# Kernel tuning notes

Measured on AMD Instinct MI355X. Metric: run time of the kernel, lower is better.

Reference implementation:

```python
import jax, jax.numpy as jnp
import numpy as np

N_HEAD = 16
N_KV_HEAD = 4
HEAD_DIM = 128
EPS = 1e-6


def apply_rotary_emb(x, cos, sin):
    # x: (B,T,H,hd); cos/sin: (1,T,1,hd//2)
    d = x.shape[3] // 2
    x1, x2 = x[..., :d], x[..., d:]
    y1 = x1 * cos + x2 * sin
    y2 = x1 * -sin + x2 * cos
    return jnp.concatenate([y1, y2], axis=3).astype(x.dtype)


def rmsnorm(x):
    # flax nnx.RMSNorm with use_scale=False: x * rsqrt(mean(x^2) + eps)
    ms = jnp.mean(jnp.square(x), axis=-1, keepdims=True)
    return (x * jax.lax.rsqrt(ms + EPS)).astype(x.dtype)


def setup_inputs() -> dict:
    key = jax.random.key(0)
    ks = jax.random.split(key, 7)
    B, T, C = 4, 2048, 2048
    s = 0.02
    return {
        "x": jax.random.normal(ks[0], (B, T, C), jnp.float32),
        "cos": jax.random.normal(ks[1], (1, T, 1, HEAD_DIM // 2), jnp.float32),
        "sin": jax.random.normal(ks[2], (1, T, 1, HEAD_DIM // 2), jnp.float32),
        "Wq": jax.random.normal(ks[3], (C, N_HEAD * HEAD_DIM), jnp.float32) * s,
        "Wk": jax.random.normal(ks[4], (C, N_KV_HEAD * HEAD_DIM), jnp.float32) * s,
        "Wv": jax.random.normal(ks[5], (C, N_KV_HEAD * HEAD_DIM), jnp.float32) * s,
        "Wo": jax.random.normal(ks[6], (C, C), jnp.float32) * s,
    }


def reference(x, cos, sin, Wq, Wk, Wv, Wo):
    B, T, C = x.shape
    q = (x @ Wq).reshape(B, T, N_HEAD, HEAD_DIM)
    k = (x @ Wk).reshape(B, T, N_KV_HEAD, HEAD_DIM)
    v = (x @ Wv).reshape(B, T, N_KV_HEAD, HEAD_DIM)
    q = rmsnorm(apply_rotary_emb(q, cos, sin))
    k = rmsnorm(apply_rotary_emb(k, cos, sin))
    # (B,H,T,hd)
    q = jnp.transpose(q, (0, 2, 1, 3))
    k = jnp.transpose(k, (0, 2, 1, 3))
    v = jnp.transpose(v, (0, 2, 1, 3))
    nrep = N_HEAD // N_KV_HEAD
    k = jnp.repeat(k, nrep, axis=1)
    v = jnp.repeat(v, nrep, axis=1)
    scale = 1.0 / jnp.sqrt(jnp.float32(HEAD_DIM))
    att = jnp.einsum('bhqd,bhkd->bhqk', q, k) * scale
    mask = jnp.tril(jnp.ones((T, T), dtype=bool))[None, None, :, :]
    att = jnp.where(mask, att, -jnp.inf)
    att = jax.nn.softmax(att, axis=-1)
    y = jnp.einsum('bhqk,bhkd->bhqd', att, v)
    y = jnp.transpose(y, (0, 2, 1, 3)).reshape(B, T, -1)
    return y @ Wo
```

## Files before the change

kernel.cpp:

```cpp
#include <hip/hip_runtime.h>
#include <hip/hip_bf16.h>

typedef __attribute__((ext_vector_type(8))) short short8;
typedef __attribute__((ext_vector_type(4))) float f32x4;

#define B_SZ 4
#define T_SEQ 2048
#define C_DIM 2048
#define NH 16
#define NKV 4
#define HD 128

__device__ __forceinline__ unsigned short f2bf(float f) {
  union { __hip_bfloat16 h; unsigned short u; } v;
  v.h = __float2bfloat16(f);
  return v.u;
}
__device__ __forceinline__ float bf2f(unsigned short u) {
  union { unsigned short u; __hip_bfloat16 h; } v;
  v.u = u;
  return __bfloat162float(v.h);
}

__device__ __forceinline__ void gload_lds16(const unsigned short* g, unsigned short* l) {
  __builtin_amdgcn_global_load_lds(
      (const __attribute__((address_space(1))) unsigned int*)g,
      (__attribute__((address_space(3))) unsigned int*)l, 16, 0, 0);
}

__global__ void cast_x(const float* __restrict__ x, unsigned short* __restrict__ xb, int n4) {
  int i = blockIdx.x * blockDim.x + threadIdx.x;
  if (i < n4) {
    float4 f = ((const float4*)x)[i];
    ushort4 u = make_ushort4(f2bf(f.x), f2bf(f.y), f2bf(f.z), f2bf(f.w));
    ((ushort4*)xb)[i] = u;
  }
}

__global__ void wtrans(const float* __restrict__ W, unsigned short* __restrict__ Wt, int K, int N) {
  __shared__ float tile[32][33];
  int k0 = blockIdx.x * 32, n0 = blockIdx.y * 32;
  int tx = threadIdx.x, ty = threadIdx.y;
#pragma unroll
  for (int i = 0; i < 4; i++)
    tile[ty + i * 8][tx] = W[(size_t)(k0 + ty + i * 8) * N + n0 + tx];
  __syncthreads();
#pragma unroll
  for (int i = 0; i < 4; i++)
    Wt[(size_t)(n0 + ty + i * 8) * K + k0 + tx] = f2bf(tile[tx][ty + i * 8]);
}

__global__ void vtrans(const unsigned short* __restrict__ qkv, unsigned short* __restrict__ Vt) {
  __shared__ unsigned short tile[32][34];
  int t0 = blockIdx.x * 32, d0 = blockIdx.y * 32;
  int b = blockIdx.z >> 2, kvh = blockIdx.z & 3;
  int tx = threadIdx.x, ty = threadIdx.y;
#pragma unroll
  for (int i = 0; i < 4; i++)
    tile[ty + i * 8][tx] =
        qkv[(size_t)(b * T_SEQ + t0 + ty + i * 8) * 3072 + 2560 + kvh * HD + d0 + tx];
  __syncthreads();
#pragma unroll
  for (int i = 0; i < 4; i++)
    Vt[((size_t)(b * NKV + kvh) * HD + d0 + ty + i * 8) * T_SEQ + t0 + tx] = tile[tx][ty + i * 8];
}

template <typename OutT>
__global__ __launch_bounds__(256, 2) void gemm_bt(const unsigned short* __restrict__ A,
                                                  const unsigned short* __restrict__ Bt,
                                                  OutT* __restrict__ Cc, int M, int N, int K) {
  __shared__ alignas(16) unsigned short lA[128 * 32];
  __shared__ alignas(16) unsigned short lB[128 * 32];
  const int tid = threadIdx.x, lane = tid & 63, wid = tid >> 6;
  const int wr = wid >> 1, wc = wid & 1;
  const size_t row0 = (size_t)blockIdx.x * 128, col0 = (size_t)blockIdx.y * 128;
  const int lr = lane >> 2, lc = (lane & 3) * 8;
  f32x4 zero = {0.f, 0.f, 0.f, 0.f};
  f32x4 acc[4][4];
#pragma unroll
  for (int m = 0; m < 4; m++)
#pragma unroll
    for (int n = 0; n < 4; n++) acc[m][n] = zero;

  for (int k0 = 0; k0 < K; k0 += 32) {
#pragma unroll
    for (int j = 0; j < 2; ++j) {
      int chunk = wid * 2 + j;
      gload_lds16(A + (row0 + chunk * 16 + lr) * K + k0 + lc, lA + chunk * 512);
      gload_lds16(Bt + (col0 + chunk * 16 + lr) * K + k0 + lc, lB + chunk * 512);
    }
    __syncthreads();
    short8 af[4], bfr[4];
#pragma unroll
    for (int m = 0; m < 4; m++)
      af[m] = *(const short8*)(lA + (wr * 64 + m * 16 + (lane & 15)) * 32 + (lane >> 4) * 8);
#pragma unroll
    for (int n = 0; n < 4; n++)
      bfr[n] = *(const short8*)(lB + (wc * 64 + n * 16 + (lane & 15)) * 32 + (lane >> 4) * 8);
#pragma unroll
    for (int m = 0; m < 4; m++)
#pragma unroll
      for (int n = 0; n < 4; n++)
        acc[m][n] = __builtin_amdgcn_mfma_f32_16x16x32_bf16(af[m], bfr[n], acc[m][n], 0, 0, 0);
    __syncthreads();
  }
#pragma unroll
  for (int m = 0; m < 4; m++) {
#pragma unroll
    for (int n = 0; n < 4; n++) {
      size_t r = row0 + wr * 64 + m * 16 + (lane >> 4) * 4;
      size_t c = col0 + wc * 64 + n * 16 + (lane & 15);
#pragma unroll
      for (int j = 0; j < 4; j++) {
        if constexpr (sizeof(OutT) == 2)
          Cc[(r + j) * N + c] = f2bf(acc[m][n][j]);
        else
          Cc[(r + j) * N + c] = acc[m][n][j];
      }
    }
  }
}

template <int NHEADS>
__global__ void ropenorm(const unsigned short* __restrict__ qkv, int colbase,
                         const float* __restrict__ cosp, const float* __restrict__ sinp,
                         unsigned short* __restrict__ qout, float outscale) {
  int gid = blockIdx.x * 4 + (threadIdx.x >> 6);
  int lane = threadIdx.x & 63;
  int h = gid % NHEADS;
  int bt = gid / NHEADS;
  int t = bt % T_SEQ, b = bt / T_SEQ;
  const unsigned short* src = qkv + (size_t)(b * T_SEQ + t) * 3072 + colbase + h * HD;
  float x1 = bf2f(src[lane]), x2 = bf2f(src[64 + lane]);
  float c = cosp[t * 64 + lane], s = sinp[t * 64 + lane];
  float y1 = x1 * c + x2 * s;
  float y2 = x2 * c - x1 * s;
  float ss = y1 * y1 + y2 * y2;
#pragma unroll
  for (int d = 1; d < 64; d <<= 1) ss += __shfl_xor(ss, d);
  float r = rsqrtf(ss * (1.f / 128.f) + 1e-6f) * outscale;
  unsigned short* dst = qout + ((size_t)(b * NHEADS + h) * T_SEQ + t) * HD;
  dst[lane] = f2bf(y1 * r);
  dst[64 + lane] = f2bf(y2 * r);
}

__global__ __launch_bounds__(256, 2) void attn(const unsigned short* __restrict__ Qn,
                                               const unsigned short* __restrict__ Kn,
                                               const unsigned short* __restrict__ Vt,
                                               unsigned short* __restrict__ Y) {
  __shared__ alignas(16) unsigned short lK[2][64 * 128];
  __shared__ alignas(16) unsigned short lV[2][128 * 64];
  __shared__ alignas(16) unsigned short pl[4][32 * 64];

  int lin = blockIdx.x;
  int low3 = lin & 7, rest = lin >> 3;
  int chi = rest >> 6, idx = rest & 63;
  int c = (chi << 3) | low3;
  int b = c >> 2, kvh = c & 3;
  int h = kvh * 4 + (idx >> 4);
  int qt = idx & 15;
  int Q0 = qt * 128;

  int lane = threadIdx.x & 63, w = threadIdx.x >> 6;
  const int r16 = lane & 15, q4 = lane >> 4;
  const unsigned short* Qp = Qn + ((size_t)(b * NH + h) * T_SEQ + Q0 + w * 32) * HD;
  const unsigned short* Kp = Kn + (size_t)(b * NKV + kvh) * T_SEQ * HD;
  const unsigned short* Vp = Vt + (size_t)(b * NKV + kvh) * HD * T_SEQ;

  short8 qf[2][4];
#pragma unroll
  for (int m = 0; m < 2; m++)
#pragma unroll
    for (int i = 0; i < 4; i++)
      qf[m][i] = *(const short8*)(Qp + (m * 16 + r16) * HD + i * 32 + q4 * 8);

  f32x4 zero = {0.f, 0.f, 0.f, 0.f};
  f32x4 o[2][8];
  float mrow[2][4], lrow[2][4];
#pragma unroll
  for (int m = 0; m < 2; m++) {
#pragma unroll
    for (int nb = 0; nb < 8; nb++) o[m][nb] = zero;
#pragma unroll
    for (int j = 0; j < 4; j++) { mrow[m][j] = -1e30f; lrow[m][j] = 0.f; }
  }

  auto stageK = [&](int kv0, int buf) {
#pragma unroll
    for (int j = 0; j < 4; ++j) {
      int cw = w * 4 + j;
      int row = cw * 4 + (lane >> 4);
      int cb = lane & 15;
      gload_lds16(Kp + (size_t)(kv0 + row) * HD + ((cb ^ (row & 7)) * 8), &lK[buf][cw * 512]);
    }
  };
  auto stageV = [&](int kv0, int buf) {
#pragma unroll
    for (int j = 0; j < 4; ++j) {
      int cw = w * 4 + j;
      int row = cw * 8 + (lane >> 3);
      int db = lane & 7;
      gload_lds16(Vp + (size_t)row * T_SEQ + kv0 + ((db ^ (row & 7)) * 8), &lV[buf][cw * 512]);
    }
  };

  const int ntiles = 2 * qt + 2;
  const int ntw = (Q0 + w * 32 + 95) >> 6;

  stageK(0, 0);
  stageV(0, 0);
  __syncthreads();
  int cur = 0;

  for (int t = 0; t < ntiles; ++t) {
    int kv0 = t * 64;
    if (t + 1 < ntiles) { stageK(kv0 + 64, cur ^ 1); stageV(kv0 + 64, cur ^ 1); }
    if (t < ntw) {
      f32x4 s[2][4];
#pragma unroll
      for (int nt = 0; nt < 4; nt++) {
        f32x4 a0 = zero, a1 = zero;
        int krow = nt * 16 + r16;
#pragma unroll
        for (int i = 0; i < 4; i++) {
          short8 kf =
              *(const short8*)(&lK[cur][krow * 128 + ((q4 * 8 + i * 32) ^ ((krow & 7) << 3))]);
          a0 = __builtin_amdgcn_mfma_f32_16x16x32_bf16(qf[0][i], kf, a0, 0, 0, 0);
          a1 = __builtin_amdgcn_mfma_f32_16x16x32_bf16(qf[1][i], kf, a1, 0, 0, 0);
        }
        s[0][nt] = a0;
        s[1][nt] = a1;
      }
      if (kv0 + 63 > Q0 + w * 32) {
#pragma unroll
        for (int m = 0; m < 2; m++)
#pragma unroll
          for (int nt = 0; nt < 4; nt++)
#pragma unroll
            for (int j = 0; j < 4; j++) {
              int col = kv0 + nt * 16 + r16;
              int row = Q0 + w * 32 + m * 16 + q4 * 4 + j;
              if (col > row) s[m][nt][j] = -1e30f;
            }
      }
#pragma unroll
      for (int m = 0; m < 2; m++) {
        float alpha[4];
#pragma unroll
        for (int j = 0; j < 4; j++) {
          float v = fmaxf(fmaxf(s[m][0][j], s[m][1][j]), fmaxf(s[m][2][j], s[m][3][j]));
#pragma unroll
          for (int d = 1; d < 16; d <<= 1) v = fmaxf(v, __shfl_xor(v, d));
          float mn = fmaxf(mrow[m][j], v);
          alpha[j] = __expf(mrow[m][j] - mn);
          mrow[m][j] = mn;
        }
        float rs[4] = {0.f, 0.f, 0.f, 0.f};
#pragma unroll
        for (int nt = 0; nt < 4; nt++)
#pragma unroll
          for (int j = 0; j < 4; j++) {
            float p = __expf(s[m][nt][j] - mrow[m][j]);
            s[m][nt][j] = p;
            rs[j] += p;
          }
#pragma unroll
        for (int j = 0; j < 4; j++) {
          float v = rs[j];
#pragma unroll
          for (int d = 1; d < 16; d <<= 1) v += __shfl_xor(v, d);
          lrow[m][j] = lrow[m][j] * alpha[j] + v;
        }
#pragma unroll
        for (int nb = 0; nb < 8; nb++)
#pragma unroll
          for (int j = 0; j < 4; j++) o[m][nb][j] *= alpha[j];
#pragma unroll
        for (int nt = 0; nt < 4; nt++)
#pragma unroll
          for (int j = 0; j < 4; j++) {
            int prow = m * 16 + q4 * 4 + j;
            pl[w][prow * 64 + ((nt * 16 + r16) ^ ((prow & 7) << 3))] = f2bf(s[m][nt][j]);
          }
      }
#pragma unroll
      for (int ks = 0; ks < 2; ks++) {
        int t0 = ks * 32 + q4 * 8;
        int prow0 = r16, prow1 = 16 + r16;
        short8 pf0 = *(const short8*)(&pl[w][prow0 * 64 + (t0 ^ ((prow0 & 7) << 3))]);
        short8 pf1 = *(const short8*)(&pl[w][prow1 * 64 + (t0 ^ ((prow1 & 7) << 3))]);
#pragma unroll
        for (int nb = 0; nb < 8; nb++) {
          int vrow = nb * 16 + r16;
          short8 vf = *(const short8*)(&lV[cur][vrow * 64 + (t0 ^ ((vrow & 7) << 3))]);
          o[0][nb] = __builtin_amdgcn_mfma_f32_16x16x32_bf16(pf0, vf, o[0][nb], 0, 0, 0);
          o[1][nb] = __builtin_amdgcn_mfma_f32_16x16x32_bf16(pf1, vf, o[1][nb], 0, 0, 0);
        }
      }
    }
    __syncthreads();
    cur ^= 1;
  }

#pragma unroll
  for (int m = 0; m < 2; m++) {
#pragma unroll
    for (int j = 0; j < 4; j++) lrow[m][j] = 1.f / lrow[m][j];
#pragma unroll
    for (int nb = 0; nb < 8; nb++)
#pragma unroll
      for (int j = 0; j < 4; j++) {
        size_t row = (size_t)Q0 + w * 32 + m * 16 + q4 * 4 + j;
        Y[((size_t)(b * T_SEQ) + row) * (NH * HD) + h * HD + nb * 16 + r16] =
            f2bf(o[m][nb][j] * lrow[m][j]);
      }
  }
}

extern "C" void kernel_launch(void* const* d_in, const int* in_sizes, int n_in,
                              void* d_out, int out_size, void* d_ws, size_t ws_size,
                              hipStream_t stream) {
  const float* x = (const float*)d_in[0];
  const float* cosp = (const float*)d_in[1];
  const float* sinp = (const float*)d_in[2];
  const float* Wq = (const float*)d_in[3];
  const float* Wk = (const float*)d_in[4];
  const float* Wv = (const float*)d_in[5];
  const float* Wo = (const float*)d_in[6];
  float* out = (float*)d_out;

  char* ws = (char*)d_ws;
  size_t off = 0;
  auto alloc = [&](size_t bytes) { void* p = ws + off; off += bytes; return p; };
  const size_t BT = (size_t)B_SZ * T_SEQ;
  unsigned short* xb = (unsigned short*)alloc(BT * C_DIM * 2);
  unsigned short* WqkvT = (unsigned short*)alloc((size_t)3072 * 2048 * 2);
  unsigned short* WoT = (unsigned short*)alloc((size_t)2048 * 2048 * 2);
  unsigned short* qkv = (unsigned short*)alloc(BT * 3072 * 2);
  unsigned short* Kb = (unsigned short*)alloc(BT * 512 * 2);
  unsigned short* Vb = (unsigned short*)alloc(BT * 512 * 2);
  unsigned short* Qb = xb;
  unsigned short* Yb = qkv;

  dim3 tb(32, 8);
  cast_x<<<16384, 256, 0, stream>>>(x, xb, (int)(BT * C_DIM / 4));
  wtrans<<<dim3(64, 64), tb, 0, stream>>>(Wq, WqkvT, 2048, 2048);
  wtrans<<<dim3(64, 16), tb, 0, stream>>>(Wk, WqkvT + (size_t)2048 * 2048, 2048, 512);
  wtrans<<<dim3(64, 16), tb, 0, stream>>>(Wv, WqkvT + (size_t)2560 * 2048, 2048, 512);
  wtrans<<<dim3(64, 64), tb, 0, stream>>>(Wo, WoT, 2048, 2048);

  gemm_bt<unsigned short><<<dim3(64, 24), 256, 0, stream>>>(xb, WqkvT, qkv, 8192, 3072, 2048);

  ropenorm<NH><<<(B_SZ * T_SEQ * NH) / 4, 256, 0, stream>>>(qkv, 0, cosp, sinp, Qb,
                                                            0.08838834764831845f);
  ropenorm<NKV><<<(B_SZ * T_SEQ * NKV) / 4, 256, 0, stream>>>(qkv, 2048, cosp, sinp, Kb, 1.0f);
  vtrans<<<dim3(64, 4, 16), tb, 0, stream>>>(qkv, Vb);

  attn<<<dim3(1024), 256, 0, stream>>>(Qb, Kb, Vb, Yb);

  gemm_bt<float><<<dim3(64, 16), 256, 0, stream>>>(Yb, WoT, out, 8192, 2048, 2048);
}
```

Measured before the change: 465.3 us.

## Restructure attention softmax with lazy rescaling, deferred row sums, reversed tile order

Reworks the online softmax in the attention kernel. The row max is reduced across all rows at once, and the running max and accumulator are only rescaled when some row's max grows by more than a threshold. Per-lane partial row sums are kept through the loop and reduced across lanes only at the end. The change also reverses the query-tile order so the longest causal blocks are scheduled first, adds s_setprio around the MFMA sections, and changes the swizzle of the P buffer in LDS to cut bank conflicts. Together these aim to remove per-tile shuffle reductions and rescale multiplies and to improve load balance, at the risk of larger exp arguments when rescaling is skipped.

Result: faster. 442.2 us (-5.0%).

```diff
diff --git a/kernel.cpp b/kernel.cpp
--- a/kernel.cpp
+++ b/kernel.cpp
@@ -144,6 +144,10 @@
   dst[64 + lane] = f2bf(y2 * r);
 }
 
+__device__ __forceinline__ int swzP(int row) {
+  return (row & 7) ^ (((row >> 3) & 1) << 1);
+}
+
 __global__ __launch_bounds__(256, 2) void attn(const unsigned short* __restrict__ Qn,
                                                const unsigned short* __restrict__ Kn,
                                                const unsigned short* __restrict__ Vt,
@@ -158,7 +162,7 @@
   int c = (chi << 3) | low3;
   int b = c >> 2, kvh = c & 3;
   int h = kvh * 4 + (idx >> 4);
-  int qt = idx & 15;
+  int qt = 15 - (idx & 15);
   int Q0 = qt * 128;
 
   int lane = threadIdx.x & 63, w = threadIdx.x >> 6;
@@ -176,13 +180,13 @@
 
   f32x4 zero = {0.f, 0.f, 0.f, 0.f};
   f32x4 o[2][8];
-  float mrow[2][4], lrow[2][4];
+  float mrow[2][4], Lp[2][4];
 #pragma unroll
   for (int m = 0; m < 2; m++) {
 #pragma unroll
     for (int nb = 0; nb < 8; nb++) o[m][nb] = zero;
 #pragma unroll
-    for (int j = 0; j < 4; j++) { mrow[m][j] = -1e30f; lrow[m][j] = 0.f; }
+    for (int j = 0; j < 4; j++) { mrow[m][j] = -1e30f; Lp[m][j] = 0.f; }
   }
 
   auto stageK = [&](int kv0, int buf) {
@@ -217,6 +221,7 @@
     if (t + 1 < ntiles) { stageK(kv0 + 64, cur ^ 1); stageV(kv0 + 64, cur ^ 1); }
     if (t < ntw) {
       f32x4 s[2][4];
+      __builtin_amdgcn_s_setprio(1);
 #pragma unroll
       for (int nt = 0; nt < 4; nt++) {
         f32x4 a0 = zero, a1 = zero;
@@ -231,6 +236,7 @@
         s[0][nt] = a0;
         s[1][nt] = a1;
       }
+      __builtin_amdgcn_s_setprio(0);
       if (kv0 + 63 > Q0 + w * 32) {
 #pragma unroll
         for (int m = 0; m < 2; m++)
@@ -243,52 +249,54 @@
               if (col > row) s[m][nt][j] = -1e30f;
             }
       }
-#pragma unroll
-      for (int m = 0; m < 2; m++) {
-        float alpha[4];
-#pragma unroll
-        for (int j = 0; j < 4; j++) {
-          float v = fmaxf(fmaxf(s[m][0][j], s[m][1][j]), fmaxf(s[m][2][j], s[m][3][j]));
-#pragma unroll
-          for (int d = 1; d < 16; d <<= 1) v = fmaxf(v, __shfl_xor(v, d));
-          float mn = fmaxf(mrow[m][j], v);
-          alpha[j] = __expf(mrow[m][j] - mn);
-          mrow[m][j] = mn;
-        }
-        float rs[4] = {0.f, 0.f, 0.f, 0.f};
+      float pm[2][4];
+#pragma unroll
+      for (int m = 0; m < 2; m++)
+#pragma unroll
+        for (int j = 0; j < 4; j++)
+          pm[m][j] = fmaxf(fmaxf(s[m][0][j], s[m][1][j]), fmaxf(s[m][2][j], s[m][3][j]));
+#pragma unroll
+      for (int d = 1; d < 16; d <<= 1)
+#pragma unroll
+        for (int m = 0; m < 2; m++)
+#pragma unroll
+          for (int j = 0; j < 4; j++) pm[m][j] = fmaxf(pm[m][j], __shfl_xor(pm[m][j], d));
+      float dmax = -1e30f;
+#pragma unroll
+      for (int m = 0; m < 2; m++)
+#pragma unroll
+        for (int j = 0; j < 4; j++) dmax = fmaxf(dmax, pm[m][j] - mrow[m][j]);
+      if (!__all(dmax <= 8.0f)) {
+#pragma unroll
+        for (int m = 0; m < 2; m++)
+#pragma unroll
+          for (int j = 0; j < 4; j++) {
+            float mn = fmaxf(mrow[m][j], pm[m][j]);
+            float al = __expf(mrow[m][j] - mn);
+            mrow[m][j] = mn;
+            Lp[m][j] *= al;
+#pragma unroll
+            for (int nb = 0; nb < 8; nb++) o[m][nb][j] *= al;
+          }
+      }
+#pragma unroll
+      for (int m = 0; m < 2; m++)
 #pragma unroll
         for (int nt = 0; nt < 4; nt++)
 #pragma unroll
           for (int j = 0; j < 4; j++) {
             float p = __expf(s[m][nt][j] - mrow[m][j]);
-            s[m][nt][j] = p;
-            rs[j] += p;
+            Lp[m][j] += p;
+            int prow = m * 16 + q4 * 4 + j;
+            pl[w][prow * 64 + ((nt * 16 + r16) ^ (swzP(prow) << 3))] = f2bf(p);
           }
-#pragma unroll
-        for (int j = 0; j < 4; j++) {
-          float v = rs[j];
-#pragma unroll
-          for (int d = 1; d < 16; d <<= 1) v += __shfl_xor(v, d);
-          lrow[m][j] = lrow[m][j] * alpha[j] + v;
-        }
-#pragma unroll
-        for (int nb = 0; nb < 8; nb++)
-#pragma unroll
-          for (int j = 0; j < 4; j++) o[m][nb][j] *= alpha[j];
-#pragma unroll
-        for (int nt = 0; nt < 4; nt++)
-#pragma unroll
-          for (int j = 0; j < 4; j++) {
-            int prow = m * 16 + q4 * 4 + j;
-            pl[w][prow * 64 + ((nt * 16 + r16) ^ ((prow & 7) << 3))] = f2bf(s[m][nt][j]);
-          }
-      }
+      __builtin_amdgcn_s_setprio(1);
 #pragma unroll
       for (int ks = 0; ks < 2; ks++) {
         int t0 = ks * 32 + q4 * 8;
         int prow0 = r16, prow1 = 16 + r16;
-        short8 pf0 = *(const short8*)(&pl[w][prow0 * 64 + (t0 ^ ((prow0 & 7) << 3))]);
-        short8 pf1 = *(const short8*)(&pl[w][prow1 * 64 + (t0 ^ ((prow1 & 7) << 3))]);
+        short8 pf0 = *(const short8*)(&pl[w][prow0 * 64 + (t0 ^ (swzP(prow0) << 3))]);
+        short8 pf1 = *(const short8*)(&pl[w][prow1 * 64 + (t0 ^ (swzP(prow1) << 3))]);
 #pragma unroll
         for (int nb = 0; nb < 8; nb++) {
           int vrow = nb * 16 + r16;
@@ -297,24 +305,32 @@
           o[1][nb] = __builtin_amdgcn_mfma_f32_16x16x32_bf16(pf1, vf, o[1][nb], 0, 0, 0);
         }
       }
+      __builtin_amdgcn_s_setprio(0);
     }
     __syncthreads();
     cur ^= 1;
   }
 
-#pragma unroll
-  for (int m = 0; m < 2; m++) {
-#pragma unroll
-    for (int j = 0; j < 4; j++) lrow[m][j] = 1.f / lrow[m][j];
+  float linv[2][4];
+#pragma unroll
+  for (int m = 0; m < 2; m++)
+#pragma unroll
+    for (int j = 0; j < 4; j++) {
+      float v = Lp[m][j];
+#pragma unroll
+      for (int d = 1; d < 16; d <<= 1) v += __shfl_xor(v, d);
+      linv[m][j] = 1.f / v;
+    }
+#pragma unroll
+  for (int m = 0; m < 2; m++)
 #pragma unroll
     for (int nb = 0; nb < 8; nb++)
 #pragma unroll
       for (int j = 0; j < 4; j++) {
         size_t row = (size_t)Q0 + w * 32 + m * 16 + q4 * 4 + j;
         Y[((size_t)(b * T_SEQ) + row) * (NH * HD) + h * HD + nb * 16 + r16] =
-            f2bf(o[m][nb][j] * lrow[m][j]);
-      }
-  }
+            f2bf(o[m][nb][j] * linv[m][j]);
+      }
 }
 
 extern "C" void kernel_launch(void* const* d_in, const int* in_sizes, int n_in,
```
